# Optimization experiments

Measured on AMD Instinct MI355X. Metric: run time of the kernel, lower is better.

Reference implementation:

```python
import jax, jax.numpy as jnp
import numpy as np

N = 50000      # nodes
E = 1600000    # edges
M = 2          # modalities
DIN, H1, LAT, DEC, HID, NC = 2000, 500, 128, 64, 64, 16
EPS = 1e-5


def setup_inputs() -> dict:
    key = jax.random.key(0)
    ks = jax.random.split(key, 24)
    s = 0.02
    return {
        "x": jax.random.normal(ks[0], (M, N, DIN), jnp.float32),
        "src": jax.random.randint(ks[1], (E,), 0, N, jnp.int32),
        "dst": jax.random.randint(ks[2], (E,), 0, N, jnp.int32),
        "W1": jax.random.normal(ks[3], (M, DIN, H1), jnp.float32) * s,
        "b1": jax.random.normal(ks[4], (M, H1), jnp.float32) * s,
        "g1": jax.random.uniform(ks[5], (M, H1), jnp.float32) + 0.5,
        "be1": jax.random.normal(ks[6], (M, H1), jnp.float32) * s,
        "m1": jax.random.normal(ks[7], (M, H1), jnp.float32) * s,
        "v1": jax.random.uniform(ks[8], (M, H1), jnp.float32) + 0.5,
        "W2": jax.random.normal(ks[9], (M, H1, LAT), jnp.float32) * s,
        "b2": jax.random.normal(ks[10], (M, LAT), jnp.float32) * s,
        "g2": jax.random.uniform(ks[11], (M, LAT), jnp.float32) + 0.5,
        "be2": jax.random.normal(ks[12], (M, LAT), jnp.float32) * s,
        "m2": jax.random.normal(ks[13], (M, LAT), jnp.float32) * s,
        "v2": jax.random.uniform(ks[14], (M, LAT), jnp.float32) + 0.5,
        "Wd": jax.random.normal(ks[15], (M, LAT, DEC), jnp.float32) * s,
        "bd": jax.random.normal(ks[16], (M, DEC), jnp.float32) * s,
        "Wg1": jax.random.normal(ks[17], (DEC, HID), jnp.float32) * s,
        "bg1": jax.random.normal(ks[18], (HID,), jnp.float32) * s,
        "Wg2": jax.random.normal(ks[19], (HID, NC), jnp.float32) * s,
        "bg2": jax.random.normal(ks[20], (NC,), jnp.float32) * s,
    }


def _bn(h, g, b, m, v):
    # inference-mode BatchNorm1d; params broadcast over [M, 1, F]
    return (h - m[:, None, :]) * jax.lax.rsqrt(v[:, None, :] + EPS) * g[:, None, :] + b[:, None, :]


def reference(x, src, dst, W1, b1, g1, be1, m1, v1, W2, b2, g2, be2, m2, v2,
              Wd, bd, Wg1, bg1, Wg2, bg2):
    # --- multi-modal encoders (dropout = identity at eval) ---
    h = jnp.einsum('mnd,mdh->mnh', x, W1) + b1[:, None, :]        # [M,N,500]
    h = _bn(h, g1, be1, m1, v1)
    h = jnp.einsum('mnh,mhl->mnl', h, W2) + b2[:, None, :]        # [M,N,LAT]
    h = _bn(h, g2, be2, m2, v2)
    dec = jnp.einsum('mnl,mld->mnd', h, Wd) + bd[:, None, :]      # [M,N,DEC]
    node_features = jnp.mean(dec, axis=0)                         # [N,DEC]

    # --- GraphConv (DGL norm='both'): D_out^{-1/2} on src, D_in^{-1/2} on dst ---
    ones = jnp.ones(src.shape[0], jnp.float32)
    deg_out = jax.ops.segment_sum(ones, src, num_segments=N)
    deg_in = jax.ops.segment_sum(ones, dst, num_segments=N)
    c_src = jax.lax.rsqrt(jnp.clip(deg_out, 1.0))[:, None]
    c_dst = jax.lax.rsqrt(jnp.clip(deg_in, 1.0))[:, None]

    def gconv(feat, W, b):
        msg = (feat * c_src)[src]                                 # [E,F]
        agg = jax.ops.segment_sum(msg, dst, num_segments=N)       # [N,F]
        return (agg * c_dst) @ W + b

    h = jax.nn.relu(gconv(node_features, Wg1, bg1))               # [N,HID]
    score = gconv(h, Wg2, bg2)                                    # [N,NC]
    return score
```

## Files before the change

### kernel.cpp

```cpp
#include <hip/hip_runtime.h>

#define NN 50000
#define EE 1600000
#define MM 2
#define DIN 2000
#define H1 500
#define LAT 128
#define DECF 64
#define HIDF 64
#define NCF 16
#define KTOT (MM*DIN)
#define KSTEPS (KTOT/32)
#define EPSBN 1e-5f

typedef float f32x4 __attribute__((ext_vector_type(4)));
typedef short short8v __attribute__((ext_vector_type(8)));

__device__ __forceinline__ unsigned int pkbf(float a, float b){
  unsigned int ua = __float_as_uint(a), ub = __float_as_uint(b);
  ua = (ua + 0x7FFFu + ((ua>>16)&1u)) >> 16;
  ub = (ub + 0x7FFFu + ((ub>>16)&1u)) & 0xFFFF0000u;
  return ua | ub;
}

__global__ void prep0(const float* b1,const float* g1,const float* be1,const float* m1,const float* v1,
                      const float* b2,const float* g2,const float* be2,const float* m2,const float* v2,
                      float* a1,float* c1,float* a2,float* c2){
  for (int i = threadIdx.x; i < MM*H1; i += blockDim.x){
    float a = g1[i]*rsqrtf(v1[i]+EPSBN);
    a1[i]=a; c1[i]=(b1[i]-m1[i])*a+be1[i];
  }
  for (int i = threadIdx.x; i < MM*LAT; i += blockDim.x){
    float a = g2[i]*rsqrtf(v2[i]+EPSBN);
    a2[i]=a; c2[i]=(b2[i]-m2[i])*a+be2[i];
  }
}

__global__ void prep1(const float* __restrict__ W2,const float* __restrict__ Wd,
                      const float* __restrict__ a2, float* __restrict__ T){
  int g = blockIdx.x*blockDim.x + threadIdx.x;
  if (g >= MM*H1*DECF) return;
  int d = g & 63; int mk = g >> 6; int k = mk % H1; int m = mk / H1;
  const float* w2 = W2 + (size_t)(m*H1 + k)*LAT;
  const float* wd = Wd + (size_t)m*LAT*DECF + d;
  const float* a  = a2 + m*LAT;
  float acc = 0.f;
  for (int l = 0; l < LAT; ++l) acc += w2[l]*a[l]*wd[(size_t)l*DECF];
  T[g] = acc;
}

__global__ void prep2(const float* __restrict__ W1,const float* __restrict__ a1,
                      const float* __restrict__ T, unsigned short* __restrict__ WB){
  int g = blockIdx.x*blockDim.x + threadIdx.x;
  if (g >= MM*DIN*DECF) return;
  int d = g & 63; int mi = g >> 6; int i = mi % DIN; int m = mi / DIN;
  const float* w1 = W1 + (size_t)(m*DIN + i)*H1;
  const float* a  = a1 + m*H1;
  const float* t  = T + (size_t)m*H1*DECF + d;
  float acc = 0.f;
  for (int k = 0; k < H1; ++k) acc += w1[k]*a[k]*t[(size_t)k*DECF];
  acc *= 0.5f;
  unsigned int u = __float_as_uint(acc);
  unsigned short bf = (unsigned short)((u + 0x7FFFu + ((u>>16)&1u)) >> 16);
  int kc = m*DIN + i;
  int s = kc >> 5, kl = kc & 31;
  int laneB = ((kl>>3)<<4) | (d & 15);
  int t4 = d >> 4;
  WB[((size_t)((s*4 + t4)*64 + laneB))*8 + (kl & 7)] = bf;
}

__global__ void prep3(const float* __restrict__ c1,const float* __restrict__ c2,
                      const float* __restrict__ T,const float* __restrict__ Wd,
                      const float* __restrict__ bd, float* __restrict__ cbar){
  int d = threadIdx.x;
  if (d >= DECF) return;
  float s = 0.f;
  for (int m = 0; m < MM; ++m){
    float sm = bd[m*DECF + d];
    const float* t = T + (size_t)m*H1*DECF + d;
    const float* c1m = c1 + m*H1;
    for (int k = 0; k < H1; ++k) sm += c1m[k]*t[(size_t)k*DECF];
    const float* wd = Wd + (size_t)m*LAT*DECF + d;
    const float* c2m = c2 + m*LAT;
    for (int l = 0; l < LAT; ++l) sm += c2m[l]*wd[(size_t)l*DECF];
    s += sm;
  }
  cbar[d] = 0.5f*s;
}

__global__ void degk(const int* __restrict__ src,const int* __restrict__ dst,
                     int* __restrict__ dout,int* __restrict__ din){
  int e = blockIdx.x*blockDim.x + threadIdx.x;
  if (e >= EE) return;
  atomicAdd(&dout[src[e]], 1);
  atomicAdd(&din[dst[e]], 1);
}

__global__ void normk(const int* __restrict__ dout,const int* __restrict__ din,
                      float* __restrict__ csrc,float* __restrict__ cdst){
  int n = blockIdx.x*blockDim.x + threadIdx.x;
  if (n >= NN) return;
  int a = dout[n]; if (a < 1) a = 1;
  int b = din[n];  if (b < 1) b = 1;
  csrc[n] = rsqrtf((float)a);
  cdst[n] = rsqrtf((float)b);
}

__global__ __launch_bounds__(1024) void scan1(const int* __restrict__ deg, int* __restrict__ rp,
                      int* __restrict__ bsum, int n){
  __shared__ int sm[1024];
  int i = blockIdx.x*1024 + threadIdx.x;
  int v = (i < n) ? deg[i] : 0;
  sm[threadIdx.x] = v; __syncthreads();
  for (int off=1; off<1024; off<<=1){
    int t = (threadIdx.x >= off) ? sm[threadIdx.x-off] : 0;
    __syncthreads();
    sm[threadIdx.x] += t;
    __syncthreads();
  }
  if (i < n) rp[i] = sm[threadIdx.x] - v;
  if (threadIdx.x == 1023) bsum[blockIdx.x] = sm[1023];
}

__global__ void scan2(const int* __restrict__ bsum, int* __restrict__ boff, int nb,
                      int* __restrict__ rp, int n){
  if (threadIdx.x==0 && blockIdx.x==0){
    int run = 0;
    for (int b=0;b<nb;b++){ boff[b]=run; run+=bsum[b]; }
    rp[n] = run;
  }
}

__global__ void scan3(int* __restrict__ rp, const int* __restrict__ boff, int n){
  int i = blockIdx.x*blockDim.x + threadIdx.x;
  if (i < n) rp[i] += boff[i>>10];
}

__global__ void scatk(const int* __restrict__ src,const int* __restrict__ dst,
                      const int* __restrict__ rp,int* __restrict__ cur,int* __restrict__ ss){
  int e = blockIdx.x*blockDim.x + threadIdx.x;
  if (e >= EE) return;
  int d = dst[e];
  int p = rp[d] + atomicAdd(&cur[d], 1);
  ss[p] = src[e];
}

__global__ __launch_bounds__(256) void gemm_nf(
    const float* __restrict__ x, const short8v* __restrict__ WB,
    const float* __restrict__ cbar, const float* __restrict__ csrc,
    float* __restrict__ nfpre)
{
  const int lane = threadIdx.x & 63;
  const int wave = threadIdx.x >> 6;
  const int n0 = blockIdx.x*64 + wave*16;
  const int r = lane & 15;
  const int kg = (lane >> 4) << 3;
  int row = n0 + r; if (row > NN-1) row = NN-1;
  const float* xrow = x + (size_t)row * DIN;

  f32x4 acc0 = {0.f,0.f,0.f,0.f}, acc1 = acc0, acc2 = acc0, acc3 = acc0;

  f32x4 A0c, A1c; short8v B0c, B1c, B2c, B3c;
  {
    const float* p = xrow + kg;
    A0c = *(const f32x4*)p; A1c = *(const f32x4*)(p+4);
    const short8v* bp = WB + lane;
    B0c = bp[0]; B1c = bp[64]; B2c = bp[128]; B3c = bp[192];
  }
  for (int s = 0; s < KSTEPS-1; ++s){
    f32x4 A0n, A1n; short8v B0n, B1n, B2n, B3n;
    {
      int kr = (s+1)*32 + kg;
      const float* p = (kr < DIN) ? (xrow + kr)
                                  : (xrow + (size_t)(NN-1)*DIN + kr);
      A0n = *(const f32x4*)p; A1n = *(const f32x4*)(p+4);
      const short8v* bp = WB + (size_t)(s+1)*256 + lane;
      B0n = bp[0]; B1n = bp[64]; B2n = bp[128]; B3n = bp[192];
    }
    union { short8v v; unsigned int u[4]; } AF;
    AF.u[0]=pkbf(A0c[0],A0c[1]); AF.u[1]=pkbf(A0c[2],A0c[3]);
    AF.u[2]=pkbf(A1c[0],A1c[1]); AF.u[3]=pkbf(A1c[2],A1c[3]);
    acc0 = __builtin_amdgcn_mfma_f32_16x16x32_bf16(AF.v, B0c, acc0, 0,0,0);
    acc1 = __builtin_amdgcn_mfma_f32_16x16x32_bf16(AF.v, B1c, acc1, 0,0,0);
    acc2 = __builtin_amdgcn_mfma_f32_16x16x32_bf16(AF.v, B2c, acc2, 0,0,0);
    acc3 = __builtin_amdgcn_mfma_f32_16x16x32_bf16(AF.v, B3c, acc3, 0,0,0);
    A0c=A0n; A1c=A1n; B0c=B0n; B1c=B1n; B2c=B2n; B3c=B3n;
  }
  {
    union { short8v v; unsigned int u[4]; } AF;
    AF.u[0]=pkbf(A0c[0],A0c[1]); AF.u[1]=pkbf(A0c[2],A0c[3]);
    AF.u[2]=pkbf(A1c[0],A1c[1]); AF.u[3]=pkbf(A1c[2],A1c[3]);
    acc0 = __builtin_amdgcn_mfma_f32_16x16x32_bf16(AF.v, B0c, acc0, 0,0,0);
    acc1 = __builtin_amdgcn_mfma_f32_16x16x32_bf16(AF.v, B1c, acc1, 0,0,0);
    acc2 = __builtin_amdgcn_mfma_f32_16x16x32_bf16(AF.v, B2c, acc2, 0,0,0);
    acc3 = __builtin_amdgcn_mfma_f32_16x16x32_bf16(AF.v, B3c, acc3, 0,0,0);
  }
  const int rg = (lane >> 4) << 2;
  float cb0 = cbar[r], cb1 = cbar[16+r], cb2 = cbar[32+r], cb3 = cbar[48+r];
  #pragma unroll
  for (int rr = 0; rr < 4; ++rr){
    int rowD = n0 + rg + rr;
    if (rowD < NN){
      float cs = csrc[rowD];
      float* o = nfpre + (size_t)rowD*64 + r;
      o[0]  = (acc0[rr] + cb0)*cs;
      o[16] = (acc1[rr] + cb1)*cs;
      o[32] = (acc2[rr] + cb2)*cs;
      o[48] = (acc3[rr] + cb3)*cs;
    }
  }
}

__global__ __launch_bounds__(256) void gath(const float* __restrict__ feat,const int* __restrict__ rp,
                     const int* __restrict__ ss, float* __restrict__ out){
  int wid = (blockIdx.x*blockDim.x + threadIdx.x) >> 6;
  int lane = threadIdx.x & 63;
  if (wid >= NN) return;
  int beg = rp[wid], end = rp[wid+1];
  float s = 0.f;
  int e = beg;
  for (; e + 4 <= end; e += 4){
    int i0=ss[e], i1=ss[e+1], i2=ss[e+2], i3=ss[e+3];
    float f0=feat[(size_t)i0*64+lane], f1=feat[(size_t)i1*64+lane],
          f2=feat[(size_t)i2*64+lane], f3=feat[(size_t)i3*64+lane];
    s += f0+f1+f2+f3;
  }
  for (; e < end; ++e) s += feat[(size_t)ss[e]*64+lane];
  out[(size_t)wid*64+lane] = s;
}

__global__ __launch_bounds__(256) void dense1(const float* __restrict__ gat,const float* __restrict__ Wg1,
                       const float* __restrict__ bg1,const float* __restrict__ csrc,
                       const float* __restrict__ cdst,float* __restrict__ hpre){
  __shared__ float W[64*64];
  for (int i = threadIdx.x; i < 64*64; i += 256) W[i] = Wg1[i];
  __syncthreads();
  int wave = threadIdx.x >> 6, lane = threadIdx.x & 63;
  int n = blockIdx.x*4 + wave;
  if (n >= NN) return;
  float g = gat[(size_t)n*64 + lane];
  float acc = 0.f;
  #pragma unroll
  for (int k = 0; k < 64; ++k)
    acc += __shfl(g, k, 64) * W[k*64 + lane];
  float h = fmaxf(cdst[n]*acc + bg1[lane], 0.f) * csrc[n];
  hpre[(size_t)n*64 + lane] = h;
}

__global__ __launch_bounds__(256) void dense2(const float* __restrict__ gat,const float* __restrict__ Wg2,
                       const float* __restrict__ bg2,const float* __restrict__ cdst,
                       float* __restrict__ score){
  __shared__ float W[64*16];
  for (int i = threadIdx.x; i < 64*16; i += 256) W[i] = Wg2[i];
  __syncthreads();
  int wave = threadIdx.x >> 6, lane = threadIdx.x & 63;
  int n = blockIdx.x*4 + wave;
  if (n >= NN) return;
  float g = gat[(size_t)n*64 + lane];
  int c = lane & 15;
  float acc = 0.f;
  #pragma unroll
  for (int k = 0; k < 64; ++k)
    acc += __shfl(g, k, 64) * W[k*16 + c];
  if (lane < 16) score[(size_t)n*16 + lane] = cdst[n]*acc + bg2[lane];
}

extern "C" void kernel_launch(void* const* d_in, const int* in_sizes, int n_in,
                              void* d_out, int out_size, void* d_ws, size_t ws_size,
                              hipStream_t stream){
  const float* x   = (const float*)d_in[0];
  const int* src   = (const int*)d_in[1];
  const int* dst   = (const int*)d_in[2];
  const float* W1  = (const float*)d_in[3];
  const float* b1  = (const float*)d_in[4];
  const float* g1  = (const float*)d_in[5];
  const float* be1 = (const float*)d_in[6];
  const float* m1  = (const float*)d_in[7];
  const float* v1  = (const float*)d_in[8];
  const float* W2  = (const float*)d_in[9];
  const float* b2  = (const float*)d_in[10];
  const float* g2  = (const float*)d_in[11];
  const float* be2 = (const float*)d_in[12];
  const float* m2  = (const float*)d_in[13];
  const float* v2  = (const float*)d_in[14];
  const float* Wd  = (const float*)d_in[15];
  const float* bd  = (const float*)d_in[16];
  const float* Wg1 = (const float*)d_in[17];
  const float* bg1 = (const float*)d_in[18];
  const float* Wg2 = (const float*)d_in[19];
  const float* bg2 = (const float*)d_in[20];
  float* score = (float*)d_out;

  char* w = (char*)d_ws;
  size_t off = 0;
  auto alc = [&](size_t b){ size_t c = off; off += (b + 255) & ~(size_t)255; return c; };
  size_t o_dout = alc((size_t)NN*4), o_din = alc((size_t)NN*4), o_cur = alc((size_t)NN*4);
  size_t o_rp  = alc((size_t)(NN+1)*4), o_bsum = alc(256*4), o_boff = alc(256*4);
  size_t o_csrc = alc((size_t)NN*4), o_cdst = alc((size_t)NN*4);
  size_t o_a1 = alc((size_t)MM*H1*4), o_c1 = alc((size_t)MM*H1*4);
  size_t o_a2 = alc((size_t)MM*LAT*4), o_c2 = alc((size_t)MM*LAT*4);
  size_t o_T = alc((size_t)MM*H1*DECF*4), o_cbar = alc(DECF*4);
  size_t o_WB = alc((size_t)MM*DIN*DECF*2);
  size_t o_ss = alc((size_t)EE*4);
  size_t o_nf = alc((size_t)NN*64*4);
  size_t o_g  = alc((size_t)NN*64*4);

  int* dout = (int*)(w+o_dout); int* din = (int*)(w+o_din); int* cur = (int*)(w+o_cur);
  int* rp = (int*)(w+o_rp); int* bsum = (int*)(w+o_bsum); int* boff = (int*)(w+o_boff);
  float* csrc = (float*)(w+o_csrc); float* cdst = (float*)(w+o_cdst);
  float* a1 = (float*)(w+o_a1); float* c1 = (float*)(w+o_c1);
  float* a2 = (float*)(w+o_a2); float* c2 = (float*)(w+o_c2);
  float* T = (float*)(w+o_T); float* cbar = (float*)(w+o_cbar);
  unsigned short* WBu = (unsigned short*)(w+o_WB);
  int* ss = (int*)(w+o_ss);
  float* nf = (float*)(w+o_nf); float* gbuf = (float*)(w+o_g);

  hipMemsetAsync(dout, 0, (size_t)NN*4, stream);
  hipMemsetAsync(din, 0, (size_t)NN*4, stream);
  hipMemsetAsync(cur, 0, (size_t)NN*4, stream);

  prep0<<<1,256,0,stream>>>(b1,g1,be1,m1,v1,b2,g2,be2,m2,v2,a1,c1,a2,c2);
  prep1<<<(MM*H1*DECF+255)/256,256,0,stream>>>(W2,Wd,a2,T);
  prep2<<<(MM*DIN*DECF+255)/256,256,0,stream>>>(W1,a1,T,WBu);
  prep3<<<1,64,0,stream>>>(c1,c2,T,Wd,bd,cbar);

  degk<<<(EE+255)/256,256,0,stream>>>(src,dst,dout,din);
  normk<<<(NN+255)/256,256,0,stream>>>(dout,din,csrc,cdst);
  int nb = (NN+1023)/1024;
  scan1<<<nb,1024,0,stream>>>(din,rp,bsum,NN);
  scan2<<<1,1,0,stream>>>(bsum,boff,nb,rp,NN);
  scan3<<<(NN+255)/256,256,0,stream>>>(rp,boff,NN);
  scatk<<<(EE+255)/256,256,0,stream>>>(src,dst,rp,cur,ss);

  gemm_nf<<<(NN+63)/64,256,0,stream>>>(x,(const short8v*)(w+o_WB),cbar,csrc,nf);

  gath<<<(NN*64+255)/256,256,0,stream>>>(nf,rp,ss,gbuf);
  dense1<<<(NN+3)/4,256,0,stream>>>(gbuf,Wg1,bg1,csrc,cdst,nf);
  gath<<<(NN*64+255)/256,256,0,stream>>>(nf,rp,ss,gbuf);
  dense2<<<(NN+3)/4,256,0,stream>>>(gbuf,Wg2,bg2,cdst,score);
}
```

Baseline: 866.7 us.

## Fuse gather with dense layers, merge prep and scan kernels, vectorize gathers

Fuses each CSR gather with its following dense layer so the aggregated features stay in registers instead of going through a global buffer. The gather now loads float4 per lane with four edges in flight per wave, then reduces across lane groups with shuffles. The BN prep kernels are folded into their consumers, and the scan and normalization steps merge into a single kernel that sums block totals per thread. The three memsets collapse into one. Together these cut the number of kernel launches and global round-trips, at the cost of some redundant per-thread work (recomputed rsqrt, the serial bsum loop).

```diff
diff --git a/kernel.cpp b/kernel.cpp
--- a/kernel.cpp
+++ b/kernel.cpp
@@ -7,8 +7,6 @@
 #define H1 500
 #define LAT 128
 #define DECF 64
-#define HIDF 64
-#define NCF 16
 #define KTOT (MM*DIN)
 #define KSTEPS (KTOT/32)
 #define EPSBN 1e-5f
@@ -23,42 +21,37 @@
   return ua | ub;
 }
 
-__global__ void prep0(const float* b1,const float* g1,const float* be1,const float* m1,const float* v1,
-                      const float* b2,const float* g2,const float* be2,const float* m2,const float* v2,
-                      float* a1,float* c1,float* a2,float* c2){
-  for (int i = threadIdx.x; i < MM*H1; i += blockDim.x){
-    float a = g1[i]*rsqrtf(v1[i]+EPSBN);
-    a1[i]=a; c1[i]=(b1[i]-m1[i])*a+be1[i];
-  }
-  for (int i = threadIdx.x; i < MM*LAT; i += blockDim.x){
-    float a = g2[i]*rsqrtf(v2[i]+EPSBN);
-    a2[i]=a; c2[i]=(b2[i]-m2[i])*a+be2[i];
-  }
-}
-
-__global__ void prep1(const float* __restrict__ W2,const float* __restrict__ Wd,
-                      const float* __restrict__ a2, float* __restrict__ T){
-  int g = blockIdx.x*blockDim.x + threadIdx.x;
-  if (g >= MM*H1*DECF) return;
-  int d = g & 63; int mk = g >> 6; int k = mk % H1; int m = mk / H1;
+__global__ __launch_bounds__(256) void prepA(const float* __restrict__ W2,const float* __restrict__ Wd,
+                      const float* __restrict__ g2,const float* __restrict__ v2,
+                      float* __restrict__ T){
+  __shared__ float a2[LAT];
+  int m = (blockIdx.x*4) / H1;
+  if (threadIdx.x < LAT)
+    a2[threadIdx.x] = g2[m*LAT+threadIdx.x]*rsqrtf(v2[m*LAT+threadIdx.x]+EPSBN);
+  __syncthreads();
+  int g = blockIdx.x*256 + threadIdx.x;
+  int d = g & 63; int mk = g >> 6; int k = mk % H1;
   const float* w2 = W2 + (size_t)(m*H1 + k)*LAT;
   const float* wd = Wd + (size_t)m*LAT*DECF + d;
-  const float* a  = a2 + m*LAT;
   float acc = 0.f;
-  for (int l = 0; l < LAT; ++l) acc += w2[l]*a[l]*wd[(size_t)l*DECF];
+  for (int l = 0; l < LAT; ++l) acc += w2[l]*a2[l]*wd[(size_t)l*DECF];
   T[g] = acc;
 }
 
-__global__ void prep2(const float* __restrict__ W1,const float* __restrict__ a1,
-                      const float* __restrict__ T, unsigned short* __restrict__ WB){
-  int g = blockIdx.x*blockDim.x + threadIdx.x;
-  if (g >= MM*DIN*DECF) return;
-  int d = g & 63; int mi = g >> 6; int i = mi % DIN; int m = mi / DIN;
+__global__ __launch_bounds__(256) void prepB(const float* __restrict__ W1,const float* __restrict__ g1,
+                      const float* __restrict__ v1,const float* __restrict__ T,
+                      unsigned short* __restrict__ WB){
+  __shared__ float a1[H1];
+  int m = (blockIdx.x*4) / DIN;
+  for (int k = threadIdx.x; k < H1; k += 256)
+    a1[k] = g1[m*H1+k]*rsqrtf(v1[m*H1+k]+EPSBN);
+  __syncthreads();
+  int g = blockIdx.x*256 + threadIdx.x;
+  int d = g & 63; int mi = g >> 6; int i = mi % DIN;
   const float* w1 = W1 + (size_t)(m*DIN + i)*H1;
-  const float* a  = a1 + m*H1;
   const float* t  = T + (size_t)m*H1*DECF + d;
   float acc = 0.f;
-  for (int k = 0; k < H1; ++k) acc += w1[k]*a[k]*t[(size_t)k*DECF];
+  for (int k = 0; k < H1; ++k) acc += w1[k]*a1[k]*t[(size_t)k*DECF];
   acc *= 0.5f;
   unsigned int u = __float_as_uint(acc);
   unsigned short bf = (unsigned short)((u + 0x7FFFu + ((u>>16)&1u)) >> 16);
@@ -69,7 +62,10 @@
   WB[((size_t)((s*4 + t4)*64 + laneB))*8 + (kl & 7)] = bf;
 }
 
-__global__ void prep3(const float* __restrict__ c1,const float* __restrict__ c2,
+__global__ void prepC(const float* __restrict__ b1,const float* __restrict__ g1,const float* __restrict__ be1,
+                      const float* __restrict__ m1,const float* __restrict__ v1,
+                      const float* __restrict__ b2,const float* __restrict__ g2,const float* __restrict__ be2,
+                      const float* __restrict__ m2,const float* __restrict__ v2,
                       const float* __restrict__ T,const float* __restrict__ Wd,
                       const float* __restrict__ bd, float* __restrict__ cbar){
   int d = threadIdx.x;
@@ -78,11 +74,17 @@
   for (int m = 0; m < MM; ++m){
     float sm = bd[m*DECF + d];
     const float* t = T + (size_t)m*H1*DECF + d;
-    const float* c1m = c1 + m*H1;
-    for (int k = 0; k < H1; ++k) sm += c1m[k]*t[(size_t)k*DECF];
+    for (int k = 0; k < H1; ++k){
+      float a = g1[m*H1+k]*rsqrtf(v1[m*H1+k]+EPSBN);
+      float c = (b1[m*H1+k]-m1[m*H1+k])*a + be1[m*H1+k];
+      sm += c*t[(size_t)k*DECF];
+    }
     const float* wd = Wd + (size_t)m*LAT*DECF + d;
-    const float* c2m = c2 + m*LAT;
-    for (int l = 0; l < LAT; ++l) sm += c2m[l]*wd[(size_t)l*DECF];
+    for (int l = 0; l < LAT; ++l){
+      float a = g2[m*LAT+l]*rsqrtf(v2[m*LAT+l]+EPSBN);
+      float c = (b2[m*LAT+l]-m2[m*LAT+l])*a + be2[m*LAT+l];
+      sm += c*wd[(size_t)l*DECF];
+    }
     s += sm;
   }
   cbar[d] = 0.5f*s;
@@ -94,16 +96,6 @@
   if (e >= EE) return;
   atomicAdd(&dout[src[e]], 1);
   atomicAdd(&din[dst[e]], 1);
-}
-
-__global__ void normk(const int* __restrict__ dout,const int* __restrict__ din,
-                      float* __restrict__ csrc,float* __restrict__ cdst){
-  int n = blockIdx.x*blockDim.x + threadIdx.x;
-  if (n >= NN) return;
-  int a = dout[n]; if (a < 1) a = 1;
-  int b = din[n];  if (b < 1) b = 1;
-  csrc[n] = rsqrtf((float)a);
-  cdst[n] = rsqrtf((float)b);
 }
 
 __global__ __launch_bounds__(1024) void scan1(const int* __restrict__ deg, int* __restrict__ rp,
@@ -122,18 +114,20 @@
   if (threadIdx.x == 1023) bsum[blockIdx.x] = sm[1023];
 }
 
-__global__ void scan2(const int* __restrict__ bsum, int* __restrict__ boff, int nb,
-                      int* __restrict__ rp, int n){
-  if (threadIdx.x==0 && blockIdx.x==0){
-    int run = 0;
-    for (int b=0;b<nb;b++){ boff[b]=run; run+=bsum[b]; }
-    rp[n] = run;
-  }
-}
-
-__global__ void scan3(int* __restrict__ rp, const int* __restrict__ boff, int n){
+__global__ void scan3n(int* __restrict__ rp, const int* __restrict__ bsum,
+                       const int* __restrict__ dout, const int* __restrict__ din,
+                       float* __restrict__ csrc, float* __restrict__ cdst){
   int i = blockIdx.x*blockDim.x + threadIdx.x;
-  if (i < n) rp[i] += boff[i>>10];
+  if (i >= NN) return;
+  int b = i >> 10;
+  int base = 0;
+  for (int j = 0; j < b; ++j) base += bsum[j];
+  rp[i] += base;
+  if (i == NN-1) rp[NN] = EE;
+  int a = dout[i]; if (a < 1) a = 1;
+  int dd = din[i]; if (dd < 1) dd = 1;
+  csrc[i] = rsqrtf((float)a);
+  cdst[i] = rsqrtf((float)dd);
 }
 
 __global__ void scatk(const int* __restrict__ src,const int* __restrict__ dst,
@@ -211,57 +205,79 @@
   }
 }
 
-__global__ __launch_bounds__(256) void gath(const float* __restrict__ feat,const int* __restrict__ rp,
-                     const int* __restrict__ ss, float* __restrict__ out){
-  int wid = (blockIdx.x*blockDim.x + threadIdx.x) >> 6;
-  int lane = threadIdx.x & 63;
-  if (wid >= NN) return;
-  int beg = rp[wid], end = rp[wid+1];
-  float s = 0.f;
-  int e = beg;
-  for (; e + 4 <= end; e += 4){
-    int i0=ss[e], i1=ss[e+1], i2=ss[e+2], i3=ss[e+3];
-    float f0=feat[(size_t)i0*64+lane], f1=feat[(size_t)i1*64+lane],
-          f2=feat[(size_t)i2*64+lane], f3=feat[(size_t)i3*64+lane];
-    s += f0+f1+f2+f3;
-  }
-  for (; e < end; ++e) s += feat[(size_t)ss[e]*64+lane];
-  out[(size_t)wid*64+lane] = s;
-}
-
-__global__ __launch_bounds__(256) void dense1(const float* __restrict__ gat,const float* __restrict__ Wg1,
-                       const float* __restrict__ bg1,const float* __restrict__ csrc,
-                       const float* __restrict__ cdst,float* __restrict__ hpre){
+__global__ __launch_bounds__(256) void fgd1(const float* __restrict__ nf,const int* __restrict__ rp,
+                      const int* __restrict__ ss,const float* __restrict__ Wg1,
+                      const float* __restrict__ bg1,const float* __restrict__ csrc,
+                      const float* __restrict__ cdst,float* __restrict__ hpre){
   __shared__ float W[64*64];
   for (int i = threadIdx.x; i < 64*64; i += 256) W[i] = Wg1[i];
   __syncthreads();
   int wave = threadIdx.x >> 6, lane = threadIdx.x & 63;
   int n = blockIdx.x*4 + wave;
   if (n >= NN) return;
-  float g = gat[(size_t)n*64 + lane];
+  int q = lane >> 4, c0 = (lane & 15)*4;
+  int beg = rp[n], end = rp[n+1];
+  f32x4 s4 = {0.f,0.f,0.f,0.f};
+  int e = beg + q;
+  for (; e + 4 < end; e += 8){
+    int i0 = ss[e], i1 = ss[e+4];
+    f32x4 f0 = *(const f32x4*)(nf + (size_t)i0*64 + c0);
+    f32x4 f1 = *(const f32x4*)(nf + (size_t)i1*64 + c0);
+    s4 += f0 + f1;
+  }
+  if (e < end)
+    s4 += *(const f32x4*)(nf + (size_t)ss[e]*64 + c0);
+  s4.x += __shfl_xor(s4.x,16); s4.y += __shfl_xor(s4.y,16);
+  s4.z += __shfl_xor(s4.z,16); s4.w += __shfl_xor(s4.w,16);
+  s4.x += __shfl_xor(s4.x,32); s4.y += __shfl_xor(s4.y,32);
+  s4.z += __shfl_xor(s4.z,32); s4.w += __shfl_xor(s4.w,32);
   float acc = 0.f;
   #pragma unroll
-  for (int k = 0; k < 64; ++k)
-    acc += __shfl(g, k, 64) * W[k*64 + lane];
+  for (int l16 = 0; l16 < 16; ++l16){
+    acc += __shfl(s4.x,l16) * W[(4*l16+0)*64 + lane];
+    acc += __shfl(s4.y,l16) * W[(4*l16+1)*64 + lane];
+    acc += __shfl(s4.z,l16) * W[(4*l16+2)*64 + lane];
+    acc += __shfl(s4.w,l16) * W[(4*l16+3)*64 + lane];
+  }
   float h = fmaxf(cdst[n]*acc + bg1[lane], 0.f) * csrc[n];
   hpre[(size_t)n*64 + lane] = h;
 }
 
-__global__ __launch_bounds__(256) void dense2(const float* __restrict__ gat,const float* __restrict__ Wg2,
-                       const float* __restrict__ bg2,const float* __restrict__ cdst,
-                       float* __restrict__ score){
+__global__ __launch_bounds__(256) void fgd2(const float* __restrict__ hp,const int* __restrict__ rp,
+                      const int* __restrict__ ss,const float* __restrict__ Wg2,
+                      const float* __restrict__ bg2,const float* __restrict__ cdst,
+                      float* __restrict__ score){
   __shared__ float W[64*16];
   for (int i = threadIdx.x; i < 64*16; i += 256) W[i] = Wg2[i];
   __syncthreads();
   int wave = threadIdx.x >> 6, lane = threadIdx.x & 63;
   int n = blockIdx.x*4 + wave;
   if (n >= NN) return;
-  float g = gat[(size_t)n*64 + lane];
+  int q = lane >> 4, c0 = (lane & 15)*4;
+  int beg = rp[n], end = rp[n+1];
+  f32x4 s4 = {0.f,0.f,0.f,0.f};
+  int e = beg + q;
+  for (; e + 4 < end; e += 8){
+    int i0 = ss[e], i1 = ss[e+4];
+    f32x4 f0 = *(const f32x4*)(hp + (size_t)i0*64 + c0);
+    f32x4 f1 = *(const f32x4*)(hp + (size_t)i1*64 + c0);
+    s4 += f0 + f1;
+  }
+  if (e < end)
+    s4 += *(const f32x4*)(hp + (size_t)ss[e]*64 + c0);
+  s4.x += __shfl_xor(s4.x,16); s4.y += __shfl_xor(s4.y,16);
+  s4.z += __shfl_xor(s4.z,16); s4.w += __shfl_xor(s4.w,16);
+  s4.x += __shfl_xor(s4.x,32); s4.y += __shfl_xor(s4.y,32);
+  s4.z += __shfl_xor(s4.z,32); s4.w += __shfl_xor(s4.w,32);
   int c = lane & 15;
   float acc = 0.f;
   #pragma unroll
-  for (int k = 0; k < 64; ++k)
-    acc += __shfl(g, k, 64) * W[k*16 + c];
+  for (int l16 = 0; l16 < 16; ++l16){
+    acc += __shfl(s4.x,l16) * W[(4*l16+0)*16 + c];
+    acc += __shfl(s4.y,l16) * W[(4*l16+1)*16 + c];
+    acc += __shfl(s4.z,l16) * W[(4*l16+2)*16 + c];
+    acc += __shfl(s4.w,l16) * W[(4*l16+3)*16 + c];
+  }
   if (lane < 16) score[(size_t)n*16 + lane] = cdst[n]*acc + bg2[lane];
 }
 
@@ -295,47 +311,37 @@
   size_t off = 0;
   auto alc = [&](size_t b){ size_t c = off; off += (b + 255) & ~(size_t)255; return c; };
   size_t o_dout = alc((size_t)NN*4), o_din = alc((size_t)NN*4), o_cur = alc((size_t)NN*4);
-  size_t o_rp  = alc((size_t)(NN+1)*4), o_bsum = alc(256*4), o_boff = alc(256*4);
+  size_t zspan = off;
+  size_t o_rp  = alc((size_t)(NN+1)*4), o_bsum = alc(256*4);
   size_t o_csrc = alc((size_t)NN*4), o_cdst = alc((size_t)NN*4);
-  size_t o_a1 = alc((size_t)MM*H1*4), o_c1 = alc((size_t)MM*H1*4);
-  size_t o_a2 = alc((size_t)MM*LAT*4), o_c2 = alc((size_t)MM*LAT*4);
   size_t o_T = alc((size_t)MM*H1*DECF*4), o_cbar = alc(DECF*4);
   size_t o_WB = alc((size_t)MM*DIN*DECF*2);
   size_t o_ss = alc((size_t)EE*4);
   size_t o_nf = alc((size_t)NN*64*4);
-  size_t o_g  = alc((size_t)NN*64*4);
+  size_t o_hp = alc((size_t)NN*64*4);
 
   int* dout = (int*)(w+o_dout); int* din = (int*)(w+o_din); int* cur = (int*)(w+o_cur);
-  int* rp = (int*)(w+o_rp); int* bsum = (int*)(w+o_bsum); int* boff = (int*)(w+o_boff);
+  int* rp = (int*)(w+o_rp); int* bsum = (int*)(w+o_bsum);
   float* csrc = (float*)(w+o_csrc); float* cdst = (float*)(w+o_cdst);
-  float* a1 = (float*)(w+o_a1); float* c1 = (float*)(w+o_c1);
-  float* a2 = (float*)(w+o_a2); float* c2 = (float*)(w+o_c2);
   float* T = (float*)(w+o_T); float* cbar = (float*)(w+o_cbar);
   unsigned short* WBu = (unsigned short*)(w+o_WB);
   int* ss = (int*)(w+o_ss);
-  float* nf = (float*)(w+o_nf); float* gbuf = (float*)(w+o_g);
-
-  hipMemsetAsync(dout, 0, (size_t)NN*4, stream);
-  hipMemsetAsync(din, 0, (size_t)NN*4, stream);
-  hipMemsetAsync(cur, 0, (size_t)NN*4, stream);
-
-  prep0<<<1,256,0,stream>>>(b1,g1,be1,m1,v1,b2,g2,be2,m2,v2,a1,c1,a2,c2);
-  prep1<<<(MM*H1*DECF+255)/256,256,0,stream>>>(W2,Wd,a2,T);
-  prep2<<<(MM*DIN*DECF+255)/256,256,0,stream>>>(W1,a1,T,WBu);
-  prep3<<<1,64,0,stream>>>(c1,c2,T,Wd,bd,cbar);
+  float* nf = (float*)(w+o_nf); float* hp = (float*)(w+o_hp);
+
+  hipMemsetAsync(w, 0, zspan, stream);
+
+  prepA<<<(MM*H1*DECF)/256,256,0,stream>>>(W2,Wd,g2,v2,T);
+  prepB<<<(MM*DIN*DECF)/256,256,0,stream>>>(W1,g1,v1,T,WBu);
+  prepC<<<1,64,0,stream>>>(b1,g1,be1,m1,v1,b2,g2,be2,m2,v2,T,Wd,bd,cbar);
 
   degk<<<(EE+255)/256,256,0,stream>>>(src,dst,dout,din);
-  normk<<<(NN+255)/256,256,0,stream>>>(dout,din,csrc,cdst);
   int nb = (NN+1023)/1024;
   scan1<<<nb,1024,0,stream>>>(din,rp,bsum,NN);
-  scan2<<<1,1,0,stream>>>(bsum,boff,nb,rp,NN);
-  scan3<<<(NN+255)/256,256,0,stream>>>(rp,boff,NN);
+  scan3n<<<(NN+255)/256,256,0,stream>>>(rp,bsum,dout,din,csrc,cdst);
   scatk<<<(EE+255)/256,256,0,stream>>>(src,dst,rp,cur,ss);
 
   gemm_nf<<<(NN+63)/64,256,0,stream>>>(x,(const short8v*)(w+o_WB),cbar,csrc,nf);
 
-  gath<<<(NN*64+255)/256,256,0,stream>>>(nf,rp,ss,gbuf);
-  dense1<<<(NN+3)/4,256,0,stream>>>(gbuf,Wg1,bg1,csrc,cdst,nf);
-  gath<<<(NN*64+255)/256,256,0,stream>>>(nf,rp,ss,gbuf);
-  dense2<<<(NN+3)/4,256,0,stream>>>(gbuf,Wg2,bg2,cdst,score);
-}
+  fgd1<<<(NN+3)/4,256,0,stream>>>(nf,rp,ss,Wg1,bg1,csrc,cdst,hp);
+  fgd2<<<(NN+3)/4,256,0,stream>>>(hp,rp,ss,Wg2,bg2,cdst,score);
+}
```

After: 857.7 us. No clear change (-1.0%).
